# Kernel optimization log

Measured on AMD Instinct MI355X. Metric: run time of the kernel, lower is better.

The kernel has to match this reference:

```python
import jax, jax.numpy as jnp
import numpy as np

B, T = 1, 2048
N_EMBD = 2048
N_HEAD = 16
HEAD_DIM = 128
Q_COMP = 1536
KV_COMP = 512
ROT = 64  # rotate_dim


def setup_inputs() -> dict:
    key = jax.random.key(0)
    ks = jax.random.split(key, 12)
    nrm = lambda k, shp, sc=1.0: jax.random.normal(k, shp, jnp.float32) * sc
    return {
        "x": nrm(ks[0], (B, T, N_EMBD)),
        "cos": jax.random.uniform(ks[1], (T, ROT // 2), jnp.float32),
        "sin": jax.random.uniform(ks[2], (T, ROT // 2), jnp.float32),
        "Wq_d_w": nrm(ks[3], (Q_COMP, N_EMBD), 0.02),
        "Wq_d_b": jnp.zeros((Q_COMP,), jnp.float32),
        "Wkv_d_w": nrm(ks[4], (KV_COMP, N_EMBD), 0.02),
        "Wq_u_w": nrm(ks[5], (N_HEAD * HEAD_DIM, Q_COMP), 0.02),
        "Wk_u_w": nrm(ks[6], (N_HEAD * HEAD_DIM, KV_COMP), 0.02),
        "Wv_u_w": nrm(ks[7], (N_HEAD * HEAD_DIM, KV_COMP), 0.02),
        "W_qr_w": nrm(ks[8], (N_HEAD * ROT, Q_COMP), 0.02),
        "W_kr_w": nrm(ks[9], (ROT, N_EMBD), 0.02),
        "W_out_w": nrm(ks[10], (N_EMBD, N_HEAD * HEAD_DIM), 0.02),
    }


def _rope(x, cos, sin):
    # x: [B, H, T, r]; cos/sin: [T, r//2] broadcast over batch and heads
    d = x.shape[-1] // 2
    x1, x2 = x[..., :d], x[..., d:]
    return jnp.concatenate([x1 * cos + x2 * sin, -x1 * sin + x2 * cos], axis=-1)


def reference(x, cos, sin, Wq_d_w, Wq_d_b, Wkv_d_w, Wq_u_w, Wk_u_w, Wv_u_w, W_qr_w, W_kr_w, W_out_w):
    Bn, Tn, _ = x.shape
    cq = x @ Wq_d_w.T + Wq_d_b           # [B,T,Qc] latent query
    ckv = x @ Wkv_d_w.T                  # [B,T,Kc] compressed KV latent (= K_t = V)
    Wq_u = Wq_u_w.reshape(N_HEAD, HEAD_DIM, Q_COMP)
    Wk_u = Wk_u_w.reshape(N_HEAD, HEAD_DIM, KV_COMP)
    Wv_u = Wv_u_w.reshape(N_HEAD, HEAD_DIM, KV_COMP)
    # absorbed per-head W_qk[h] = Wq_u_h^T @ Wk_u_h : [H, Qc, Kc]
    W_qk = jnp.einsum('hdq,hdk->hqk', Wq_u, Wk_u)
    Q_t = jnp.einsum('btq,hqk->bhtk', cq, W_qk)   # [B,H,T,Kc] content query in latent space
    Q_r = _rope(jnp.einsum('btq,hrq->bhtr', cq, W_qr_w.reshape(N_HEAD, ROT, Q_COMP)), cos, sin)
    K_r = _rope((x @ W_kr_w.T)[:, None], cos, sin)  # [B,1,T,R] single shared rotary key head
    Q = jnp.concatenate([Q_t, Q_r], axis=-1)        # [B,H,T,Kc+R]
    K = jnp.concatenate([ckv[:, None], K_r], axis=-1)  # [B,1,T,Kc+R]
    scale = 1.0 / np.sqrt(KV_COMP + ROT).astype(np.float32)
    scores = jnp.einsum('bhqd,bokd->bhqk', Q, K) * scale  # [B,H,T,T]
    causal = jnp.tril(jnp.ones((Tn, Tn), dtype=bool))
    scores = jnp.where(causal, scores, jnp.asarray(-1e30, scores.dtype))
    probs = jax.nn.softmax(scores, axis=-1)
    attn = jnp.einsum('bhqk,bkc->bhqc', probs, ckv)  # [B,H,T,Kc] latent attention output
    # absorbed output projection: up-project per head via Wv_u, then W_out
    heads = jnp.einsum('bhtc,hdc->bthd', attn, Wv_u).reshape(Bn, Tn, N_HEAD * HEAD_DIM)
    return heads @ W_out_w.T                          # [B,T,C]
```

## Files before the change

kernel.cpp:

```cpp
#include <hip/hip_runtime.h>
#include <math.h>
#include <stdint.h>
#include <stddef.h>

typedef __bf16 bf16;
typedef __bf16 bf16x8 __attribute__((ext_vector_type(8)));
typedef __bf16 bf16x4 __attribute__((ext_vector_type(4)));
typedef __bf16 bf16x2 __attribute__((ext_vector_type(2)));
typedef float  f32x4  __attribute__((ext_vector_type(4)));
typedef float  f32x4v __attribute__((ext_vector_type(4)));

typedef __attribute__((address_space(1))) const void* as1cv;
typedef __attribute__((address_space(3))) void*       as3v;

__device__ __forceinline__ f32x4 mfma16(bf16x8 a, bf16x8 b, f32x4 c) {
  return __builtin_amdgcn_mfma_f32_16x16x32_bf16(a, b, c, 0, 0, 0);
}

__device__ __forceinline__ void gload_lds16(const bf16* g, bf16* l) {
  __builtin_amdgcn_global_load_lds((as1cv)g, (as3v)l, 16, 0, 0);
}

struct CvtTable {
  const float* s[9];
  bf16* d[9];
  int cum[10];
};

__global__ void cvt_all(CvtTable T, int total4) {
  int i = blockIdx.x * blockDim.x + threadIdx.x;
  int stride = gridDim.x * blockDim.x;
  for (; i < total4; i += stride) {
    int k = 0;
#pragma unroll
    for (int j = 1; j < 9; ++j) k += (i >= T.cum[j]) ? 1 : 0;
    int off = i - T.cum[k];
    f32x4v v = ((const f32x4v*)T.s[k])[off];
    bf16x4 o;
    o[0] = (bf16)v[0]; o[1] = (bf16)v[1]; o[2] = (bf16)v[2]; o[3] = (bf16)v[3];
    ((bf16x4*)T.d[k])[off] = o;
  }
}

__device__ __forceinline__ void gemm_core(
    const bf16* __restrict__ A, int lda,
    const bf16* __restrict__ B, int K,
    float* __restrict__ Cf, bf16* __restrict__ Cb, int ldc,
    const float* __restrict__ bias, int bias_n, int m0, int n0)
{
  __shared__ __align__(16) bf16 Al[2][128 * 64];
  __shared__ __align__(16) bf16 Bl[2][128 * 64];
  const int tid = threadIdx.x;
  const int l = tid & 63;
  const int wid = tid >> 6;
  const int wr = wid >> 2, wc = wid & 3;
  const int lr = l & 15, lg = l >> 4;

  const int ch0 = tid, ch1 = tid + 512;
  const int ar0 = ch0 >> 3, ap0 = (ch0 & 7) ^ (ar0 & 7);
  const int ar1 = ch1 >> 3, ap1 = (ch1 & 7) ^ (ar1 & 7);
  const bf16* pA0 = A + (size_t)(m0 + ar0) * lda + ap0 * 8;
  const bf16* pA1 = A + (size_t)(m0 + ar1) * lda + ap1 * 8;
  const bf16* pB0 = B + (size_t)(n0 + ar0) * K + ap0 * 8;
  const bf16* pB1 = B + (size_t)(n0 + ar1) * K + ap1 * 8;
  bf16* dA0[2] = { &Al[0][ch0 * 8], &Al[1][ch0 * 8] };
  bf16* dA1[2] = { &Al[0][ch1 * 8], &Al[1][ch1 * 8] };
  bf16* dB0[2] = { &Bl[0][ch0 * 8], &Bl[1][ch0 * 8] };
  bf16* dB1[2] = { &Bl[0][ch1 * 8], &Bl[1][ch1 * 8] };

  auto STAGE = [&](int b) {
    gload_lds16(pA0, b ? dA0[1] : dA0[0]);
    gload_lds16(pA1, b ? dA1[1] : dA1[0]);
    gload_lds16(pB0, b ? dB0[1] : dB0[0]);
    gload_lds16(pB1, b ? dB1[1] : dB1[0]);
    pA0 += 64; pA1 += 64; pB0 += 64; pB1 += 64;
  };

  f32x4 z = {0.f, 0.f, 0.f, 0.f};
  f32x4 acc[4][2];
#pragma unroll
  for (int i = 0; i < 4; ++i)
#pragma unroll
    for (int j = 0; j < 2; ++j) acc[i][j] = z;

  STAGE(0);
  __syncthreads();
  int cur = 0;
  for (int k0 = 0; k0 < K; k0 += 64) {
    if (k0 + 64 < K) STAGE(cur ^ 1);
#pragma unroll
    for (int kk = 0; kk < 2; ++kk) {
      bf16x8 af[4], bfr[2];
#pragma unroll
      for (int i = 0; i < 4; ++i) {
        int row = wr * 64 + i * 16 + lr;
        int cq = kk * 4 + lg;
        af[i] = *(const bf16x8*)(&Al[cur][row * 64 + ((cq ^ (row & 7)) * 8)]);
      }
#pragma unroll
      for (int j = 0; j < 2; ++j) {
        int row = wc * 32 + j * 16 + lr;
        int cq = kk * 4 + lg;
        bfr[j] = *(const bf16x8*)(&Bl[cur][row * 64 + ((cq ^ (row & 7)) * 8)]);
      }
#pragma unroll
      for (int i = 0; i < 4; ++i)
#pragma unroll
        for (int j = 0; j < 2; ++j)
          acc[i][j] = mfma16(af[i], bfr[j], acc[i][j]);
    }
    __syncthreads();
    cur ^= 1;
  }

#pragma unroll
  for (int i = 0; i < 4; ++i)
#pragma unroll
    for (int j = 0; j < 2; ++j)
#pragma unroll
      for (int r = 0; r < 4; ++r) {
        int row = m0 + wr * 64 + i * 16 + lg * 4 + r;
        int col = n0 + wc * 32 + j * 16 + lr;
        float v = acc[i][j][r];
        if (bias != nullptr && col < bias_n) v += bias[col];
        if (Cf != nullptr) Cf[(size_t)row * ldc + col] = v;
        else               Cb[(size_t)row * ldc + col] = (bf16)v;
      }
}

template<bool OUTF32>
__global__ __launch_bounds__(512) void gemm_bt(
    const bf16* __restrict__ A, int lda,
    const bf16* __restrict__ B, int K,
    float* __restrict__ Cf, bf16* __restrict__ Cb, int ldc,
    const float* __restrict__ bias, int bias_n)
{
  gemm_core(A, lda, B, K, OUTF32 ? Cf : nullptr, Cb, ldc, bias, bias_n,
            blockIdx.y * 128, blockIdx.x * 128);
}

__global__ __launch_bounds__(512) void gemm_bt_dual(
    const bf16* __restrict__ A0, int lda0, const bf16* __restrict__ B0, int K0,
    bf16* __restrict__ C0, int ldc0, int nbx0,
    const bf16* __restrict__ A1, int lda1, const bf16* __restrict__ B1, int K1,
    bf16* __restrict__ C1, int ldc1, int nbx1)
{
  int bid = blockIdx.x;
  if (bid < nbx0 * 16) {
    gemm_core(A0, lda0, B0, K0, nullptr, C0, ldc0, nullptr, 0,
              (bid / nbx0) * 128, (bid % nbx0) * 128);
  } else {
    bid -= nbx0 * 16;
    gemm_core(A1, lda1, B1, K1, nullptr, C1, ldc1, nullptr, 0,
              (bid / nbx1) * 128, (bid % nbx1) * 128);
  }
}

__global__ void rope_tv(const bf16* __restrict__ QA, const bf16* __restrict__ c_all,
                        const float* __restrict__ cosb, const float* __restrict__ sinb,
                        bf16* __restrict__ Qr, bf16* __restrict__ Kr,
                        const bf16* __restrict__ KV, bf16* __restrict__ Vt)
{
  int bid = blockIdx.x;
  if (bid < 2048) {
    int t = bid;
    for (int idx = threadIdx.x; idx < 544; idx += 256) {
      if (idx < 512) {
        int h = idx >> 5, p = idx & 31;
        float x1 = (float)QA[(size_t)t * 3072 + 2048 + h * 64 + p];
        float x2 = (float)QA[(size_t)t * 3072 + 2048 + h * 64 + 32 + p];
        float c = cosb[t * 32 + p], s = sinb[t * 32 + p];
        Qr[(size_t)t * 1024 + h * 64 + p]      = (bf16)( x1 * c + x2 * s);
        Qr[(size_t)t * 1024 + h * 64 + 32 + p] = (bf16)(-x1 * s + x2 * c);
      } else {
        int p = idx - 512;
        float x1 = (float)c_all[(size_t)t * 2176 + 2048 + p];
        float x2 = (float)c_all[(size_t)t * 2176 + 2048 + 32 + p];
        float c = cosb[t * 32 + p], s = sinb[t * 32 + p];
        Kr[(size_t)t * 64 + p]      = (bf16)( x1 * c + x2 * s);
        Kr[(size_t)t * 64 + 32 + p] = (bf16)(-x1 * s + x2 * c);
      }
    }
  } else {
    __shared__ bf16 tile[32][33];
    int tb = bid - 2048;
    int t0 = (tb & 63) * 32, c0 = (tb >> 6) * 32;
    int tx = threadIdx.x & 31, ty = threadIdx.x >> 5;
#pragma unroll
    for (int r = 0; r < 4; ++r)
      tile[ty + r * 8][tx] = KV[(size_t)(t0 + ty + r * 8) * 4096 + 2048 + c0 + tx];
    __syncthreads();
#pragma unroll
    for (int r = 0; r < 4; ++r)
      Vt[(size_t)(c0 + ty + r * 8) * 2048 + t0 + tx] = tile[tx][ty + r * 8];
  }
}

__global__ __launch_bounds__(256) void attn_kernel(
    const bf16* __restrict__ QA,
    const bf16* __restrict__ Qr,
    const bf16* __restrict__ KV,
    const bf16* __restrict__ Kr,
    const bf16* __restrict__ Vt,
    bf16* __restrict__ heads)
{
  __shared__ __align__(16) bf16 Kl[2][32 * 128];
  __shared__ __align__(16) bf16 Krl[2][32 * 64];
  __shared__ __align__(16) bf16 Vl[2][128 * 32];
  __shared__ __align__(16) bf16 Pl[4][16][40];

  const int tid = threadIdx.x;
  const int l = tid & 63;
  const int wid = tid >> 6;
  const int lr = l & 15, lg = l >> 4;

  const int wg = blockIdx.x;
  const int xcd = wg & 7, inx = wg >> 3;
  const int half = inx >> 5, j = inx & 31;
  const int h = xcd * 2 + half;
  const int qb = half ? j : 31 - j;
  const int q0 = qb * 64 + wid * 16;
  const int q = q0 + lr;

  const float scale = 0.041666666666666664f;
  f32x4 z = {0.f, 0.f, 0.f, 0.f};

  const int chK0 = tid, chK1 = tid + 256;
  const int rK0 = chK0 >> 4, pK0 = chK0 & 15;
  const int rK1 = chK1 >> 4, pK1 = chK1 & 15;
  const int cbK0 = (pK0 & 8) | ((pK0 & 7) ^ (rK0 & 7));
  const int cbK1 = (pK1 & 8) | ((pK1 & 7) ^ (rK1 & 7));
  const bf16* gK0 = &KV[(size_t)rK0 * 4096 + h * 128 + cbK0 * 8];
  const bf16* gK1 = &KV[(size_t)rK1 * 4096 + h * 128 + cbK1 * 8];
  const int rKr = tid >> 3, pKr = tid & 7, cbKr = pKr ^ (rKr & 7);
  const bf16* gKr = &Kr[(size_t)rKr * 64 + cbKr * 8];
  const int chV0 = tid, chV1 = tid + 256;
  const int rV0 = chV0 >> 2, pV0 = chV0 & 3, cbV0 = pV0 ^ ((rV0 >> 1) & 3);
  const int rV1 = chV1 >> 2, pV1 = chV1 & 3, cbV1 = pV1 ^ ((rV1 >> 1) & 3);
  const bf16* gV0 = &Vt[(size_t)(h * 128 + rV0) * 2048 + cbV0 * 8];
  const bf16* gV1 = &Vt[(size_t)(h * 128 + rV1) * 2048 + cbV1 * 8];
  bf16* dK0[2] = { &Kl[0][chK0 * 8], &Kl[1][chK0 * 8] };
  bf16* dK1[2] = { &Kl[0][chK1 * 8], &Kl[1][chK1 * 8] };
  bf16* dKr[2] = { &Krl[0][tid * 8], &Krl[1][tid * 8] };
  bf16* dV0[2] = { &Vl[0][chV0 * 8], &Vl[1][chV0 * 8] };
  bf16* dV1[2] = { &Vl[0][chV1 * 8], &Vl[1][chV1 * 8] };

  auto STAGE = [&](int b) {
    gload_lds16(gK0, b ? dK0[1] : dK0[0]);
    gload_lds16(gK1, b ? dK1[1] : dK1[0]);
    gload_lds16(gKr, b ? dKr[1] : dKr[0]);
    gload_lds16(gV0, b ? dV0[1] : dV0[0]);
    gload_lds16(gV1, b ? dV1[1] : dV1[0]);
    gK0 += 32 * 4096; gK1 += 32 * 4096; gKr += 32 * 64; gV0 += 32; gV1 += 32;
  };

  bf16x8 aq[6];
#pragma unroll
  for (int kc = 0; kc < 4; ++kc)
    aq[kc] = *(const bf16x8*)&QA[(size_t)q * 3072 + h * 128 + kc * 32 + lg * 8];
#pragma unroll
  for (int kc = 4; kc < 6; ++kc)
    aq[kc] = *(const bf16x8*)&Qr[(size_t)q * 1024 + h * 64 + (kc - 4) * 32 + lg * 8];

  float m_run = -1e30f, l_run = 0.f;
  f32x4 acc[8];
#pragma unroll
  for (int c = 0; c < 8; ++c) acc[c] = z;

  const int nIter = 2 * qb + 2;
  STAGE(0);
  __syncthreads();
  int cur = 0;
  for (int st = 0; st < nIter; ++st) {
    const int s0 = st * 32;
    if (st + 1 < nIter) STAGE(cur ^ 1);
    if (s0 <= q0 + 15) {
      f32x4 sc[2];
      sc[0] = z; sc[1] = z;
#pragma unroll
      for (int t = 0; t < 2; ++t) {
        const int rr = t * 16 + lr;
#pragma unroll
        for (int kc = 0; kc < 4; ++kc) {
          int g = kc * 4 + lg;
          bf16x8 ka = *(const bf16x8*)&Kl[cur][rr * 128 + (((g & 8) | ((g & 7) ^ (rr & 7))) * 8)];
          sc[t] = mfma16(ka, aq[kc], sc[t]);
        }
#pragma unroll
        for (int kc = 4; kc < 6; ++kc) {
          int g = (kc - 4) * 4 + lg;
          bf16x8 ka = *(const bf16x8*)&Krl[cur][rr * 64 + ((g ^ (rr & 7)) * 8)];
          sc[t] = mfma16(ka, aq[kc], sc[t]);
        }
      }
      float pv[2][4];
      float mx = -1e30f;
      if (s0 + 31 > q0) {
#pragma unroll
        for (int t = 0; t < 2; ++t)
#pragma unroll
          for (int r = 0; r < 4; ++r) {
            int k = s0 + t * 16 + lg * 4 + r;
            float v = sc[t][r] * scale;
            if (k > q) v = -1e30f;
            pv[t][r] = v;
            mx = fmaxf(mx, v);
          }
      } else {
#pragma unroll
        for (int t = 0; t < 2; ++t)
#pragma unroll
          for (int r = 0; r < 4; ++r) {
            float v = sc[t][r] * scale;
            pv[t][r] = v;
            mx = fmaxf(mx, v);
          }
      }
      mx = fmaxf(mx, __shfl_xor(mx, 16, 64));
      mx = fmaxf(mx, __shfl_xor(mx, 32, 64));
      if (!__all(mx - m_run <= 8.f)) {
        float mnew = fmaxf(m_run, mx);
        float alpha = __expf(m_run - mnew);
        l_run *= alpha;
#pragma unroll
        for (int c = 0; c < 8; ++c)
#pragma unroll
          for (int r = 0; r < 4; ++r) acc[c][r] *= alpha;
        m_run = mnew;
      }
      float sum = 0.f;
#pragma unroll
      for (int t = 0; t < 2; ++t)
#pragma unroll
        for (int r = 0; r < 4; ++r) {
          float e = __expf(pv[t][r] - m_run);
          pv[t][r] = e;
          sum += e;
        }
      sum += __shfl_xor(sum, 16, 64);
      sum += __shfl_xor(sum, 32, 64);
      l_run += sum;
#pragma unroll
      for (int t = 0; t < 2; ++t)
#pragma unroll
        for (int hf = 0; hf < 2; ++hf) {
          bf16x2 w;
          w[0] = (bf16)pv[t][2 * hf];
          w[1] = (bf16)pv[t][2 * hf + 1];
          *(bf16x2*)&Pl[wid][lr][t * 16 + lg * 4 + 2 * hf] = w;
        }
      bf16x8 pa = *(const bf16x8*)&Pl[wid][lr][lg * 8];
#pragma unroll
      for (int c = 0; c < 8; ++c) {
        int rv = c * 16 + lr;
        bf16x8 va = *(const bf16x8*)&Vl[cur][rv * 32 + ((lg ^ ((rv >> 1) & 3)) * 8)];
        acc[c] = mfma16(va, pa, acc[c]);
      }
    }
    __syncthreads();
    cur ^= 1;
  }

  const float inv = 1.f / l_run;
#pragma unroll
  for (int c = 0; c < 8; ++c) {
    bf16x4 o;
#pragma unroll
    for (int r = 0; r < 4; ++r) o[r] = (bf16)(acc[c][r] * inv);
    *(bf16x4*)&heads[(size_t)q * 2048 + h * 128 + c * 16 + lg * 4] = o;
  }
}

extern "C" void kernel_launch(void* const* d_in, const int* in_sizes, int n_in,
                              void* d_out, int out_size, void* d_ws, size_t ws_size,
                              hipStream_t stream) {
  (void)in_sizes; (void)n_in; (void)out_size; (void)ws_size;
  const float* x      = (const float*)d_in[0];
  const float* cosp   = (const float*)d_in[1];
  const float* sinp   = (const float*)d_in[2];
  const float* Wq_d   = (const float*)d_in[3];
  const float* Wq_d_b = (const float*)d_in[4];
  const float* Wkv_d  = (const float*)d_in[5];
  const float* Wq_u   = (const float*)d_in[6];
  const float* Wk_u   = (const float*)d_in[7];
  const float* Wv_u   = (const float*)d_in[8];
  const float* W_qr   = (const float*)d_in[9];
  const float* W_kr   = (const float*)d_in[10];
  const float* W_out  = (const float*)d_in[11];

  char* ws = (char*)d_ws;
  size_t off = 0;
  auto alloc = [&](size_t bytes) {
    char* p = ws + off;
    off += (bytes + 255) & ~(size_t)255;
    return p;
  };
  bf16* xb    = (bf16*)alloc((size_t)2048 * 2048 * 2);
  bf16* Wcat  = (bf16*)alloc((size_t)2176 * 2048 * 2);
  bf16* c_all = (bf16*)alloc((size_t)2048 * 2176 * 2);
  bf16* Wqu   = (bf16*)alloc((size_t)3072 * 1536 * 2);
  bf16* QA    = (bf16*)alloc((size_t)2048 * 3072 * 2);
  bf16* Wkvu  = (bf16*)alloc((size_t)4096 * 512 * 2);
  bf16* KV    = (bf16*)alloc((size_t)2048 * 4096 * 2);
  bf16* Qr    = (bf16*)alloc((size_t)2048 * 1024 * 2);
  bf16* Kr    = (bf16*)alloc((size_t)2048 * 64 * 2);
  bf16* Wout  = (bf16*)alloc((size_t)2048 * 2048 * 2);
  bf16* Vt    = xb;
  bf16* heads = Wqu;

  CvtTable T;
  const float* srcs[9] = { x, Wq_d, Wkv_d, W_kr, Wq_u, W_qr, Wk_u, Wv_u, W_out };
  bf16* dsts[9] = { xb, Wcat, Wcat + (size_t)1536 * 2048, Wcat + (size_t)2048 * 2048,
                    Wqu, Wqu + (size_t)2048 * 1536, Wkvu, Wkvu + (size_t)2048 * 512, Wout };
  size_t ns[9] = { (size_t)2048 * 2048, (size_t)1536 * 2048, (size_t)512 * 2048,
                   (size_t)64 * 2048, (size_t)2048 * 1536, (size_t)1024 * 1536,
                   (size_t)2048 * 512, (size_t)2048 * 512, (size_t)2048 * 2048 };
  int cum = 0;
  for (int i = 0; i < 9; ++i) {
    T.s[i] = srcs[i]; T.d[i] = dsts[i]; T.cum[i] = cum;
    cum += (int)(ns[i] / 4);
  }
  T.cum[9] = cum;
  cvt_all<<<2048, 256, 0, stream>>>(T, cum);

  gemm_bt<false><<<dim3(17, 16), 512, 0, stream>>>(xb, 2048, Wcat, 2048,
                                                   nullptr, c_all, 2176, Wq_d_b, 1536);
  gemm_bt_dual<<<24 * 16 + 32 * 16, 512, 0, stream>>>(
      c_all, 2176, Wqu, 1536, QA, 3072, 24,
      c_all + 1536, 2176, Wkvu, 512, KV, 4096, 32);
  rope_tv<<<2048 + 4096, 256, 0, stream>>>(QA, c_all, cosp, sinp, Qr, Kr, KV, Vt);
  attn_kernel<<<512, 256, 0, stream>>>(QA, Qr, KV, Kr, Vt, heads);
  gemm_bt<true><<<dim3(16, 16), 512, 0, stream>>>(heads, 2048, Wout, 2048,
                                                  (float*)d_out, nullptr, 2048, nullptr, 0);
}
```

Measured before the change: 305.8 us.

## Shrink GEMM tiles to 64x128 with 256 threads, XCD swizzle, and MFMA setprio

Result: slower. 331.0 us (+8.2%).

```diff
diff --git a/kernel.cpp b/kernel.cpp
--- a/kernel.cpp
+++ b/kernel.cpp
@@ -21,6 +21,11 @@
   __builtin_amdgcn_global_load_lds((as1cv)g, (as3v)l, 16, 0, 0);
 }
 
+__device__ __forceinline__ int xswz(int bid, int nwg) {
+  int cpx = nwg >> 3;
+  return (bid & 7) * cpx + (bid >> 3);
+}
+
 struct CvtTable {
   const float* s[9];
   bf16* d[9];
@@ -48,32 +53,39 @@
     float* __restrict__ Cf, bf16* __restrict__ Cb, int ldc,
     const float* __restrict__ bias, int bias_n, int m0, int n0)
 {
-  __shared__ __align__(16) bf16 Al[2][128 * 64];
+  __shared__ __align__(16) bf16 Al[2][64 * 64];
   __shared__ __align__(16) bf16 Bl[2][128 * 64];
   const int tid = threadIdx.x;
   const int l = tid & 63;
-  const int wid = tid >> 6;
-  const int wr = wid >> 2, wc = wid & 3;
+  const int wc = tid >> 6;
   const int lr = l & 15, lg = l >> 4;
 
-  const int ch0 = tid, ch1 = tid + 512;
-  const int ar0 = ch0 >> 3, ap0 = (ch0 & 7) ^ (ar0 & 7);
-  const int ar1 = ch1 >> 3, ap1 = (ch1 & 7) ^ (ar1 & 7);
-  const bf16* pA0 = A + (size_t)(m0 + ar0) * lda + ap0 * 8;
-  const bf16* pA1 = A + (size_t)(m0 + ar1) * lda + ap1 * 8;
-  const bf16* pB0 = B + (size_t)(n0 + ar0) * K + ap0 * 8;
-  const bf16* pB1 = B + (size_t)(n0 + ar1) * K + ap1 * 8;
-  bf16* dA0[2] = { &Al[0][ch0 * 8], &Al[1][ch0 * 8] };
-  bf16* dA1[2] = { &Al[0][ch1 * 8], &Al[1][ch1 * 8] };
-  bf16* dB0[2] = { &Bl[0][ch0 * 8], &Bl[1][ch0 * 8] };
-  bf16* dB1[2] = { &Bl[0][ch1 * 8], &Bl[1][ch1 * 8] };
+  const int cA0 = tid, cA1 = tid + 256;
+  const int rA0 = cA0 >> 3, pA0s = (cA0 & 7) ^ (rA0 & 7);
+  const int rA1 = cA1 >> 3, pA1s = (cA1 & 7) ^ (rA1 & 7);
+  const bf16* pA0 = A + (size_t)(m0 + rA0) * lda + pA0s * 8;
+  const bf16* pA1 = A + (size_t)(m0 + rA1) * lda + pA1s * 8;
+  const bf16* pB[4];
+  bf16* dB[4][2];
+#pragma unroll
+  for (int it = 0; it < 4; ++it) {
+    int ch = it * 256 + tid;
+    int row = ch >> 3, p = (ch & 7) ^ (row & 7);
+    pB[it] = B + (size_t)(n0 + row) * K + p * 8;
+    dB[it][0] = &Bl[0][ch * 8];
+    dB[it][1] = &Bl[1][ch * 8];
+  }
+  bf16* dA0[2] = { &Al[0][cA0 * 8], &Al[1][cA0 * 8] };
+  bf16* dA1[2] = { &Al[0][cA1 * 8], &Al[1][cA1 * 8] };
 
   auto STAGE = [&](int b) {
-    gload_lds16(pA0, b ? dA0[1] : dA0[0]);
-    gload_lds16(pA1, b ? dA1[1] : dA1[0]);
-    gload_lds16(pB0, b ? dB0[1] : dB0[0]);
-    gload_lds16(pB1, b ? dB1[1] : dB1[0]);
-    pA0 += 64; pA1 += 64; pB0 += 64; pB1 += 64;
+    gload_lds16(pA0, dA0[b]);
+    gload_lds16(pA1, dA1[b]);
+#pragma unroll
+    for (int it = 0; it < 4; ++it) gload_lds16(pB[it], dB[it][b]);
+    pA0 += 64; pA1 += 64;
+#pragma unroll
+    for (int it = 0; it < 4; ++it) pB[it] += 64;
   };
 
   f32x4 z = {0.f, 0.f, 0.f, 0.f};
@@ -93,7 +105,7 @@
       bf16x8 af[4], bfr[2];
 #pragma unroll
       for (int i = 0; i < 4; ++i) {
-        int row = wr * 64 + i * 16 + lr;
+        int row = i * 16 + lr;
         int cq = kk * 4 + lg;
         af[i] = *(const bf16x8*)(&Al[cur][row * 64 + ((cq ^ (row & 7)) * 8)]);
       }
@@ -103,11 +115,13 @@
         int cq = kk * 4 + lg;
         bfr[j] = *(const bf16x8*)(&Bl[cur][row * 64 + ((cq ^ (row & 7)) * 8)]);
       }
+      __builtin_amdgcn_s_setprio(1);
 #pragma unroll
       for (int i = 0; i < 4; ++i)
 #pragma unroll
         for (int j = 0; j < 2; ++j)
           acc[i][j] = mfma16(af[i], bfr[j], acc[i][j]);
+      __builtin_amdgcn_s_setprio(0);
     }
     __syncthreads();
     cur ^= 1;
@@ -119,7 +133,7 @@
     for (int j = 0; j < 2; ++j)
 #pragma unroll
       for (int r = 0; r < 4; ++r) {
-        int row = m0 + wr * 64 + i * 16 + lg * 4 + r;
+        int row = m0 + i * 16 + lg * 4 + r;
         int col = n0 + wc * 32 + j * 16 + lr;
         float v = acc[i][j][r];
         if (bias != nullptr && col < bias_n) v += bias[col];
@@ -129,30 +143,31 @@
 }
 
 template<bool OUTF32>
-__global__ __launch_bounds__(512) void gemm_bt(
+__global__ __launch_bounds__(256) void gemm_bt(
     const bf16* __restrict__ A, int lda,
     const bf16* __restrict__ B, int K,
     float* __restrict__ Cf, bf16* __restrict__ Cb, int ldc,
-    const float* __restrict__ bias, int bias_n)
+    const float* __restrict__ bias, int bias_n, int nbx, int nwg)
 {
+  int bid = xswz(blockIdx.x, nwg);
   gemm_core(A, lda, B, K, OUTF32 ? Cf : nullptr, Cb, ldc, bias, bias_n,
-            blockIdx.y * 128, blockIdx.x * 128);
-}
-
-__global__ __launch_bounds__(512) void gemm_bt_dual(
+            (bid / nbx) * 64, (bid % nbx) * 128);
+}
+
+__global__ __launch_bounds__(256) void gemm_bt_dual(
     const bf16* __restrict__ A0, int lda0, const bf16* __restrict__ B0, int K0,
-    bf16* __restrict__ C0, int ldc0, int nbx0,
+    bf16* __restrict__ C0, int ldc0, int nbx0, int nwg0,
     const bf16* __restrict__ A1, int lda1, const bf16* __restrict__ B1, int K1,
-    bf16* __restrict__ C1, int ldc1, int nbx1)
+    bf16* __restrict__ C1, int ldc1, int nbx1, int nwgT)
 {
-  int bid = blockIdx.x;
-  if (bid < nbx0 * 16) {
+  int bid = xswz(blockIdx.x, nwgT);
+  if (bid < nwg0) {
     gemm_core(A0, lda0, B0, K0, nullptr, C0, ldc0, nullptr, 0,
-              (bid / nbx0) * 128, (bid % nbx0) * 128);
+              (bid / nbx0) * 64, (bid % nbx0) * 128);
   } else {
-    bid -= nbx0 * 16;
+    bid -= nwg0;
     gemm_core(A1, lda1, B1, K1, nullptr, C1, ldc1, nullptr, 0,
-              (bid / nbx1) * 128, (bid % nbx1) * 128);
+              (bid / nbx1) * 64, (bid % nbx1) * 128);
   }
 }
 
@@ -277,6 +292,7 @@
     if (s0 <= q0 + 15) {
       f32x4 sc[2];
       sc[0] = z; sc[1] = z;
+      __builtin_amdgcn_s_setprio(1);
 #pragma unroll
       for (int t = 0; t < 2; ++t) {
         const int rr = t * 16 + lr;
@@ -293,6 +309,7 @@
           sc[t] = mfma16(ka, aq[kc], sc[t]);
         }
       }
+      __builtin_amdgcn_s_setprio(0);
       float pv[2][4];
       float mx = -1e30f;
       if (s0 + 31 > q0) {
@@ -350,12 +367,14 @@
           *(bf16x2*)&Pl[wid][lr][t * 16 + lg * 4 + 2 * hf] = w;
         }
       bf16x8 pa = *(const bf16x8*)&Pl[wid][lr][lg * 8];
+      __builtin_amdgcn_s_setprio(1);
 #pragma unroll
       for (int c = 0; c < 8; ++c) {
         int rv = c * 16 + lr;
         bf16x8 va = *(const bf16x8*)&Vl[cur][rv * 32 + ((lg ^ ((rv >> 1) & 3)) * 8)];
         acc[c] = mfma16(va, pa, acc[c]);
       }
+      __builtin_amdgcn_s_setprio(0);
     }
     __syncthreads();
     cur ^= 1;
@@ -423,13 +442,13 @@
   T.cum[9] = cum;
   cvt_all<<<2048, 256, 0, stream>>>(T, cum);
 
-  gemm_bt<false><<<dim3(17, 16), 512, 0, stream>>>(xb, 2048, Wcat, 2048,
-                                                   nullptr, c_all, 2176, Wq_d_b, 1536);
-  gemm_bt_dual<<<24 * 16 + 32 * 16, 512, 0, stream>>>(
-      c_all, 2176, Wqu, 1536, QA, 3072, 24,
-      c_all + 1536, 2176, Wkvu, 512, KV, 4096, 32);
+  gemm_bt<false><<<544, 256, 0, stream>>>(xb, 2048, Wcat, 2048,
+                                          nullptr, c_all, 2176, Wq_d_b, 1536, 17, 544);
+  gemm_bt_dual<<<768 + 1024, 256, 0, stream>>>(
+      c_all, 2176, Wqu, 1536, QA, 3072, 24, 768,
+      c_all + 1536, 2176, Wkvu, 512, KV, 4096, 32, 1792);
   rope_tv<<<2048 + 4096, 256, 0, stream>>>(QA, c_all, cosp, sinp, Qr, Kr, KV, Vt);
   attn_kernel<<<512, 256, 0, stream>>>(QA, Qr, KV, Kr, Vt, heads);
-  gemm_bt<true><<<dim3(16, 16), 512, 0, stream>>>(heads, 2048, Wout, 2048,
-                                                  (float*)d_out, nullptr, 2048, nullptr, 0);
-}
+  gemm_bt<true><<<512, 256, 0, stream>>>(heads, 2048, Wout, 2048,
+                                         (float*)d_out, nullptr, 2048, nullptr, 0, 16, 512);
+}
```
